# Performance work log

Measured on AMD Instinct MI355X. Metric: run time of the kernel, lower is better.

## Reference

```python
import jax, jax.numpy as jnp
import numpy as np
from jax import lax

B, C, H, W = 8, 64, 64, 64
C8 = C // 8
EPS = 1e-5


def setup_inputs() -> dict:
    key = jax.random.key(0)
    ks = jax.random.split(key, 10)
    s = lambda *sh: 0.02
    inp = {
        "x": jax.random.normal(ks[0], (B, C, H, W), dtype=jnp.float32),
        "conv_b_w": jax.random.normal(ks[1], (C8, C), dtype=jnp.float32) * 0.05,
        "conv_b_b": jnp.zeros((C8,), jnp.float32),
        "conv_c_w": jax.random.normal(ks[2], (C8, C), dtype=jnp.float32) * 0.05,
        "conv_c_b": jnp.zeros((C8,), jnp.float32),
        "conv_d_w": jax.random.normal(ks[3], (C, C), dtype=jnp.float32) * 0.05,
        "conv_d_b": jnp.zeros((C,), jnp.float32),
        "alpha": jnp.zeros((1,), jnp.float32) + 0.1,  # learned PAM scale
        "beta": jnp.zeros((1,), jnp.float32) + 0.1,   # learned CAM scale
        "conv_w": jax.random.normal(ks[4], (2 * C, C, 3, 3), dtype=jnp.float32) * 0.02,
        "conv_bias": jnp.zeros((2 * C,), jnp.float32),
        "bn_gamma": jnp.ones((2 * C,), jnp.float32),
        "bn_beta": jnp.zeros((2 * C,), jnp.float32),
    }
    return inp


def _conv1x1(x, w, b):
    # x: [B,C,H,W], w: [O,C] -> [B,O,H,W]
    return jnp.einsum('oc,bchw->bohw', w, x) + b[None, :, None, None]


def _forward(x, conv_b_w, conv_b_b, conv_c_w, conv_c_b, conv_d_w, conv_d_b,
             alpha, beta, conv_w, conv_bias, bn_gamma, bn_beta):
    b, c, h, w = x.shape
    n = h * w
    # ---- Position Attention Module ----
    feat_b = _conv1x1(x, conv_b_w, conv_b_b).reshape(b, C8, n)   # [B,C8,N]
    feat_c = _conv1x1(x, conv_c_w, conv_c_b).reshape(b, C8, n)   # [B,C8,N]
    # torch: bmm(feat_b^T [B,N,C8], feat_c [B,C8,N]) -> [B,N,N]
    attn_s = jax.nn.softmax(jnp.einsum('bcn,bcm->bnm', feat_b, feat_c), axis=-1)
    feat_d = _conv1x1(x, conv_d_w, conv_d_b).reshape(b, c, n)    # [B,C,N]
    # torch: bmm(feat_d, attn_s^T) -> out[b,c,n] = sum_m feat_d[b,c,m]*attn[b,n,m]
    feat_e = jnp.einsum('bcm,bnm->bcn', feat_d, attn_s).reshape(b, c, h, w)
    x = alpha[0] * feat_e + x
    # ---- Channel Attention Module ----
    fa = x.reshape(b, c, n)                                      # [B,C,N]
    att = jnp.einsum('bcn,bdn->bcd', fa, fa)                     # [B,C,C]
    att_new = jnp.max(att, axis=-1, keepdims=True) - att
    att = jax.nn.softmax(att_new, axis=-1)
    fe = jnp.einsum('bcd,bdn->bcn', att, fa).reshape(b, c, h, w)
    x = beta[0] * fe + x
    # ---- conv3x3 + BN (batch stats) + ReLU + maxpool(2,2,pad=(1,0)) ----
    out = lax.conv_general_dilated(x, conv_w, (1, 1), ((1, 1), (1, 1)),
                                   dimension_numbers=('NCHW', 'OIHW', 'NCHW'))
    out = out + conv_bias[None, :, None, None]
    mean = jnp.mean(out, axis=(0, 2, 3), keepdims=True)
    var = jnp.var(out, axis=(0, 2, 3), keepdims=True)
    out = (out - mean) * lax.rsqrt(var + EPS)
    out = out * bn_gamma[None, :, None, None] + bn_beta[None, :, None, None]
    out = jax.nn.relu(out)
    # MaxPool2d(kernel=2, stride=2, padding=(1,0)): -inf padding on height only
    out = lax.reduce_window(out, -jnp.inf, lax.max,
                            (1, 1, 2, 2), (1, 1, 2, 2),
                            ((0, 0), (0, 0), (1, 1), (0, 0)))
    return out


def reference(x, conv_b_w, conv_b_b, conv_c_w, conv_c_b, conv_d_w, conv_d_b,
              alpha, beta, conv_w, conv_bias, bn_gamma, bn_beta):
    return _forward(x, conv_b_w, conv_b_b, conv_c_w, conv_c_b, conv_d_w, conv_d_b,
                    alpha, beta, conv_w, conv_bias, bn_gamma, bn_beta)
```

## Files before the change

kernel.cpp:

```cpp
#include <hip/hip_runtime.h>

using f32x4  = __attribute__((ext_vector_type(4))) float;
using f32x16 = __attribute__((ext_vector_type(16))) float;
using bf16x8 = __attribute__((ext_vector_type(8))) short;
using u32x4  = __attribute__((ext_vector_type(4))) unsigned int;
using u32x2  = __attribute__((ext_vector_type(2))) unsigned int;
typedef unsigned short u16;

__device__ __forceinline__ u16 f2bf(float f) {
  unsigned u = __float_as_uint(f);
  unsigned r = (u + 0x7FFFu + ((u >> 16) & 1u)) >> 16;
  return (u16)r;
}

#if __has_builtin(__builtin_amdgcn_exp2f)
#define FAST_EXP2(x) __builtin_amdgcn_exp2f(x)
#else
#define FAST_EXP2(x) __expf(0.6931471805599453f * (x))
#endif

#define LOG2E 1.4426950408889634f

__device__ __forceinline__ void permswap32(unsigned& a, unsigned& b) {
  asm volatile("v_permlane32_swap_b32 %0, %1" : "+v"(a), "+v"(b));
}

__global__ void __launch_bounds__(256) k1_conv1x1(
    const float* __restrict__ x, const float* __restrict__ wB, const float* __restrict__ bB,
    const float* __restrict__ wC, const float* __restrict__ bC,
    const float* __restrict__ wD, const float* __restrict__ bD,
    u16* __restrict__ featBb, u16* __restrict__ featCb, u16* __restrict__ featD,
    const float* __restrict__ cw, u16* __restrict__ wb) {
  const int t = threadIdx.x;
  const int b = blockIdx.y;
  const int z = blockIdx.z;
  if (z == 2) {
    int gid = (b * 16 + blockIdx.x) * 256 + t;
#pragma unroll
    for (int k = 0; k < 3; ++k) {
      int F = gid + k * 32768;
      if (F < 73728) {
        int j = F & 7, lane = (F >> 3) & 63, T = F >> 9;
        int tap = T >> 4, g = (T >> 1) & 7, kc = T & 1;
        int l16 = lane & 15, quad = lane >> 4;
        int oc = g * 16 + l16, ic = kc * 32 + quad * 8 + j;
        wb[F] = f2bf(cw[(oc * 64 + ic) * 9 + tap]);
      }
    }
    return;
  }
  __shared__ float W[2560];
  __shared__ float Bias[40];
  const int n = blockIdx.x * 256 + t;
  if (z == 0) {
    for (int i = t; i < 2560; i += 256) {
      float v;
      if (i < 512) v = wB[i];
      else if (i < 1024) v = wC[i - 512];
      else v = wD[i - 1024];
      W[i] = v;
    }
    if (t < 8) Bias[t] = bB[t];
    else if (t < 16) Bias[t] = bC[t - 8];
    else if (t < 40) Bias[t] = bD[t - 16];
  } else {
    for (int i = t; i < 2560; i += 256) W[i] = wD[1536 + i];
    if (t < 40) Bias[t] = bD[24 + t];
  }
  __syncthreads();
  float xv[64];
#pragma unroll
  for (int c = 0; c < 64; ++c) xv[c] = x[((b * 64 + c) << 12) + n];
  if (z == 0) {
    float o[16];
#pragma unroll
    for (int k = 0; k < 16; ++k) {
      f32x4 s = {0.f, 0.f, 0.f, 0.f};
#pragma unroll
      for (int cq = 0; cq < 16; ++cq) {
        f32x4 wv = *(const f32x4*)&W[k * 64 + cq * 4];
        f32x4 xq = {xv[cq * 4], xv[cq * 4 + 1], xv[cq * 4 + 2], xv[cq * 4 + 3]};
        s += wv * xq;
      }
      o[k] = Bias[k] + s[0] + s[1] + s[2] + s[3];
    }
    int base = ((b << 12) + n) * 8;
    u32x4 pb, pc;
#pragma unroll
    for (int i = 0; i < 4; ++i) {
      pb[i] = (unsigned)f2bf(o[2 * i] * LOG2E) | ((unsigned)f2bf(o[2 * i + 1] * LOG2E) << 16);
      pc[i] = (unsigned)f2bf(o[8 + 2 * i]) | ((unsigned)f2bf(o[8 + 2 * i + 1]) << 16);
    }
    *(u32x4*)&featBb[base] = pb;
    *(u32x4*)&featCb[base] = pc;
#pragma unroll 4
    for (int k = 0; k < 24; ++k) {
      f32x4 s = {0.f, 0.f, 0.f, 0.f};
#pragma unroll
      for (int cq = 0; cq < 16; ++cq) {
        f32x4 wv = *(const f32x4*)&W[1024 + k * 64 + cq * 4];
        f32x4 xq = {xv[cq * 4], xv[cq * 4 + 1], xv[cq * 4 + 2], xv[cq * 4 + 3]};
        s += wv * xq;
      }
      float val = Bias[16 + k] + s[0] + s[1] + s[2] + s[3];
      featD[((b * 64 + k) << 12) + n] = f2bf(val);
    }
  } else {
#pragma unroll 4
    for (int k = 0; k < 40; ++k) {
      f32x4 s = {0.f, 0.f, 0.f, 0.f};
#pragma unroll
      for (int cq = 0; cq < 16; ++cq) {
        f32x4 wv = *(const f32x4*)&W[k * 64 + cq * 4];
        f32x4 xq = {xv[cq * 4], xv[cq * 4 + 1], xv[cq * 4 + 2], xv[cq * 4 + 3]};
        s += wv * xq;
      }
      float val = Bias[k] + s[0] + s[1] + s[2] + s[3];
      featD[((b * 64 + 24 + k) << 12) + n] = f2bf(val);
    }
  }
}

__global__ void __launch_bounds__(256) k2_pam_part(
    const u16* __restrict__ fBb, const u16* __restrict__ fCb, const u16* __restrict__ fD,
    u16* __restrict__ numPart, float* __restrict__ denPart) {
  __shared__ u16 Df[2][64 * 132];
  const int t = threadIdx.x, b = blockIdx.y, z = blockIdx.z;
  const int w = t >> 6, lane = t & 63, l32 = lane & 31, hi = lane >> 5;
  const int nb = blockIdx.x * 128 + w * 32;
  const int mz = z << 10;

  int srow[4], smo[4];
#pragma unroll
  for (int hh = 0; hh < 4; ++hh) {
    int idx = hh * 256 + t;
    srow[hh] = idx >> 4;
    smo[hh] = (idx & 15) << 3;
  }

  bf16x8 bq = (bf16x8)(short)0;
  if (hi == 0) bq = *(const bf16x8*)&fBb[(((b << 12) + nb + l32) << 3)];

  bf16x8 onesA = (bf16x8)(short)0;
  if (l32 == 0) onesA = (bf16x8)(short)0x3F80;

  f32x16 acc0 = (f32x16)(0.0f), acc1 = (f32x16)(0.0f), accd = (f32x16)(0.0f);

  u32x4 sreg[4];
#define K2_ISSUE(CH) {                                                        \
    int m0_ = mz + ((CH) << 7);                                               \
    _Pragma("unroll")                                                         \
    for (int hh = 0; hh < 4; ++hh)                                            \
      sreg[hh] = *(const u32x4*)&fD[((b * 64 + srow[hh]) << 12) + m0_ + smo[hh]]; }
#define K2_WRITE(BUF) {                                                       \
    _Pragma("unroll")                                                         \
    for (int hh = 0; hh < 4; ++hh)                                            \
      *(u32x4*)&Df[BUF][srow[hh] * 132 + smo[hh]] = sreg[hh]; }
#define K2_AF_LOAD(DST, CH) {                                                 \
    int m0_ = mz + ((CH) << 7);                                               \
    _Pragma("unroll")                                                         \
    for (int mt2 = 0; mt2 < 4; ++mt2) {                                       \
      bf16x8 a_ = (bf16x8)(short)0;                                           \
      if (hi == 0) a_ = *(const bf16x8*)&fCb[(((b << 12) + m0_ + mt2 * 32 + l32) << 3)]; \
      DST[mt2] = a_;                                                          \
    } }

  K2_ISSUE(0);
  K2_WRITE(0);
  bf16x8 afv[4], afn[4];
  K2_AF_LOAD(afv, 0);
  __syncthreads();

#pragma unroll 2
  for (int ch = 0; ch < 8; ++ch) {
    const int cur = ch & 1;
    if (ch < 7) K2_ISSUE(ch + 1);
    if (ch < 7) K2_AF_LOAD(afn, ch + 1);

    f32x16 sc = __builtin_amdgcn_mfma_f32_32x32x16_bf16(afv[0], bq, (f32x16)(0.0f), 0, 0, 0);
#pragma unroll
    for (int mt2 = 0; mt2 < 4; ++mt2) {
      f32x16 sn;
      if (mt2 < 3) sn = __builtin_amdgcn_mfma_f32_32x32x16_bf16(afv[mt2 + 1], bq, (f32x16)(0.0f), 0, 0, 0);
      unsigned u0[8];
#pragma unroll
      for (int i = 0; i < 8; ++i) {
        float e0 = FAST_EXP2(sc[2 * i]);
        float e1 = FAST_EXP2(sc[2 * i + 1]);
        u0[i] = __builtin_amdgcn_perm(__float_as_uint(e1), __float_as_uint(e0), 0x07060302u);
      }
      permswap32(u0[0], u0[2]); permswap32(u0[1], u0[3]);
      permswap32(u0[4], u0[6]); permswap32(u0[5], u0[7]);

      __builtin_amdgcn_s_setprio(1);
#pragma unroll
      for (int kc = 0; kc < 2; ++kc) {
        u32x4 q0 = {u0[4 * kc], u0[4 * kc + 1], u0[4 * kc + 2], u0[4 * kc + 3]};
        bf16x8 bv0 = *(bf16x8*)&q0;
        bf16x8 av0 = *(const bf16x8*)&Df[cur][(l32) * 132 + mt2 * 32 + kc * 16 + hi * 8];
        bf16x8 av1 = *(const bf16x8*)&Df[cur][(32 + l32) * 132 + mt2 * 32 + kc * 16 + hi * 8];
        acc0 = __builtin_amdgcn_mfma_f32_32x32x16_bf16(av0, bv0, acc0, 0, 0, 0);
        acc1 = __builtin_amdgcn_mfma_f32_32x32x16_bf16(av1, bv0, acc1, 0, 0, 0);
        accd = __builtin_amdgcn_mfma_f32_32x32x16_bf16(onesA, bv0, accd, 0, 0, 0);
      }
      __builtin_amdgcn_s_setprio(0);
      if (mt2 < 3) sc = sn;
    }

    if (ch < 7) {
      K2_WRITE(cur ^ 1);
#pragma unroll
      for (int mt2 = 0; mt2 < 4; ++mt2) afv[mt2] = afn[mt2];
    }
    __syncthreads();
  }
#undef K2_ISSUE
#undef K2_WRITE
#undef K2_AF_LOAD

  const int zb = z * 8 + b;
#pragma unroll
  for (int r = 0; r < 16; ++r) {
    int c = (r & 3) + ((r >> 2) << 3) + (hi << 2);
    numPart[((zb * 64 + c) << 12) + nb + l32] = (u16)(__float_as_uint(acc0[r]) >> 16);
    numPart[((zb * 64 + c + 32) << 12) + nb + l32] = (u16)(__float_as_uint(acc1[r]) >> 16);
  }
  if (hi == 0) denPart[(zb << 12) + nb + l32] = accd[0];
}

__global__ void __launch_bounds__(256) k3_gram(
    const u16* __restrict__ numPart, const float* __restrict__ denPart,
    const float* __restrict__ x, const float* __restrict__ alpha,
    float* __restrict__ x1, float* __restrict__ attPart) {
  __shared__ float X[64 * 132];
  __shared__ float Dinv[128];
  const int t = threadIdx.x, b = blockIdx.y, cx = blockIdx.x, zz = blockIdx.z;
  const int n0 = cx * 128;
  if (t < 128) {
    float den = 0.f;
#pragma unroll
    for (int z = 0; z < 4; ++z) den += denPart[(((z * 8 + b) << 12)) + n0 + t];
    Dinv[t] = alpha[0] / den;
  }
  __syncthreads();
  for (int idx = t; idx < 4096; idx += 256) {
    int row = idx >> 6, cp = (idx & 63) * 2;
    int gi = ((b * 64 + row) << 12) + n0 + cp;
    float num0 = 0.f, num1 = 0.f;
#pragma unroll
    for (int z = 0; z < 4; ++z) {
      unsigned v = *(const unsigned*)&numPart[(((z * 8 + b) * 64 + row) << 12) + n0 + cp];
      num0 += __uint_as_float(v << 16);
      num1 += __uint_as_float(v & 0xFFFF0000u);
    }
    float v0 = num0 * Dinv[cp] + x[gi];
    float v1 = num1 * Dinv[cp + 1] + x[gi + 1];
    X[row * 132 + cp] = v0;
    X[row * 132 + cp + 1] = v1;
    if (zz == 0) {
      x1[gi] = v0;
      x1[gi + 1] = v1;
    }
  }
  __syncthreads();
  const int cg = t >> 4, dg = t & 15;
  const int cbase = zz * 32 + cg * 2;
  f32x4 acc[2][4];
#pragma unroll
  for (int i = 0; i < 2; ++i)
#pragma unroll
    for (int k = 0; k < 4; ++k) acc[i][k] = (f32x4){0.f, 0.f, 0.f, 0.f};
  for (int nq0 = 0; nq0 < 32; ++nq0) {
    int nq = (nq0 + dg) & 31;
    f32x4 a[2], bb[4];
#pragma unroll
    for (int i = 0; i < 2; ++i) a[i] = *(const f32x4*)&X[(cbase + i) * 132 + nq * 4];
#pragma unroll
    for (int k = 0; k < 4; ++k) bb[k] = *(const f32x4*)&X[(dg * 4 + k) * 132 + nq * 4];
#pragma unroll
    for (int i = 0; i < 2; ++i)
#pragma unroll
      for (int k = 0; k < 4; ++k) acc[i][k] += a[i] * bb[k];
  }
#pragma unroll
  for (int i = 0; i < 2; ++i)
#pragma unroll
    for (int k = 0; k < 4; ++k) {
      f32x4 s = acc[i][k];
      attPart[((b * 32 + cx) * 64 + cbase + i) * 64 + dg * 4 + k] = s[0] + s[1] + s[2] + s[3];
    }
}

__global__ void __launch_bounds__(64) k4_softmax(const float* __restrict__ attPart, float* __restrict__ attP) {
  const int b = blockIdx.y, c = blockIdx.x, d = threadIdx.x;
  float v = 0.f;
  for (int p = 0; p < 32; ++p) v += attPart[((b * 32 + p) * 64 + c) * 64 + d];
  float mn = v;
#pragma unroll
  for (int off = 1; off < 64; off <<= 1) mn = fminf(mn, __shfl_xor(mn, off));
  float e = __expf(mn - v);
  float sum = e;
#pragma unroll
  for (int off = 1; off < 64; off <<= 1) sum += __shfl_xor(sum, off);
  attP[(b * 64 + c) * 64 + d] = e / sum;
}

__global__ void __launch_bounds__(256) k5_apply(
    const float* __restrict__ attP, const float* __restrict__ x1,
    const float* __restrict__ beta, u16* __restrict__ x2b) {
  __shared__ float A[64 * 68];
  const int t = threadIdx.x, b = blockIdx.y;
  for (int idx = t; idx < 4096; idx += 256) A[(idx >> 6) * 68 + (idx & 63)] = attP[(b << 12) + idx];
  __syncthreads();
  const int n = blockIdx.x * 32 + (t & 31);
  const int cq = t >> 5;
  const float bv = beta[0];
  float acc[8];
#pragma unroll
  for (int i = 0; i < 8; ++i) acc[i] = 0.f;
  const float* xcol = x1 + ((size_t)b << 18) + n;
#pragma unroll 4
  for (int dq = 0; dq < 16; ++dq) {
    float x0 = xcol[(size_t)(dq * 4 + 0) << 12];
    float x1v = xcol[(size_t)(dq * 4 + 1) << 12];
    float x2 = xcol[(size_t)(dq * 4 + 2) << 12];
    float x3 = xcol[(size_t)(dq * 4 + 3) << 12];
#pragma unroll
    for (int i = 0; i < 8; ++i) {
      const float* av = &A[(cq * 8 + i) * 68 + dq * 4];
      acc[i] += av[0] * x0 + av[1] * x1v + av[2] * x2 + av[3] * x3;
    }
  }
  u16* orow = x2b + ((((size_t)(b << 12) + n) << 6) + cq * 8);
  unsigned pk[4];
#pragma unroll
  for (int i = 0; i < 8; i += 2) {
    float v0 = bv * acc[i] + xcol[(size_t)(cq * 8 + i) << 12];
    float v1 = bv * acc[i + 1] + xcol[(size_t)(cq * 8 + i + 1) << 12];
    pk[i >> 1] = (unsigned)f2bf(v0) | ((unsigned)f2bf(v1) << 16);
  }
  *(u32x4*)&orow[0] = (u32x4){pk[0], pk[1], pk[2], pk[3]};
}

__global__ void __launch_bounds__(256) k6_mfma(const u16* __restrict__ x2b, const u16* __restrict__ wb,
                                               float* __restrict__ y, float* __restrict__ pstat2) {
  __shared__ u16 Xl[3 * 66 * 72];
  __shared__ float pp[4][64][2];
  const int t = threadIdx.x, b = blockIdx.y, h = blockIdx.x;
  for (int idx = t; idx < 3 * 66 * 8; idx += 256) {
    int r = idx / 528;
    int rem = idx - r * 528;
    int c = rem >> 3, icq = rem & 7;
    int gy = h - 1 + r, gx = c - 1;
    u32x4 v = {0u, 0u, 0u, 0u};
    if (gy >= 0 && gy < 64 && gx >= 0 && gx < 64)
      v = *(const u32x4*)&x2b[(((size_t)(b << 6 | gy) << 6) + gx) * 64 + icq * 8];
    *(u32x4*)&Xl[(r * 66 + c) * 72 + icq * 8] = v;
  }
  __syncthreads();
  const int w = t >> 6, lane = t & 63, quad = lane >> 4, l16 = lane & 15;
  const int mBase = (w & 1) * 64;
  const int og = (w & 1) * 4;
  const int nBase = (w >> 1) * 32;
  f32x4 acc[4][2];
#pragma unroll
  for (int ot = 0; ot < 4; ++ot)
#pragma unroll
    for (int nt = 0; nt < 2; ++nt) acc[ot][nt] = (f32x4){0.f, 0.f, 0.f, 0.f};
#pragma unroll 3
  for (int tap = 0; tap < 9; ++tap) {
    const int dy = tap / 3, dx = tap - dy * 3;
    bf16x8 af[4][2];
#pragma unroll
    for (int ot = 0; ot < 4; ++ot)
#pragma unroll
      for (int kc = 0; kc < 2; ++kc)
        af[ot][kc] = *(const bf16x8*)&wb[((((tap * 8 + og + ot) * 2 + kc) << 6) + lane) << 3];
#pragma unroll
    for (int nt = 0; nt < 2; ++nt) {
      const int prow = dy * 66 + nBase + nt * 16 + l16 + dx;
#pragma unroll
      for (int kc = 0; kc < 2; ++kc) {
        bf16x8 bv = *(const bf16x8*)&Xl[prow * 72 + kc * 32 + quad * 8];
#pragma unroll
        for (int ot = 0; ot < 4; ++ot)
          acc[ot][nt] = __builtin_amdgcn_mfma_f32_16x16x32_bf16(af[ot][kc], bv, acc[ot][nt], 0, 0, 0);
      }
    }
  }
#pragma unroll
  for (int ot = 0; ot < 4; ++ot)
#pragma unroll
    for (int nt = 0; nt < 2; ++nt)
#pragma unroll
      for (int r = 0; r < 4; ++r) {
        int oc = mBase + ot * 16 + quad * 4 + r;
        int pix = nBase + nt * 16 + l16;
        y[((b * 128 + oc) << 12) + (h << 6) + pix] = acc[ot][nt][r];
      }
  float bs[4][4], bss[4][4];
#pragma unroll
  for (int ot = 0; ot < 4; ++ot)
#pragma unroll
    for (int r = 0; r < 4; ++r) {
      float v0 = acc[ot][0][r], v1 = acc[ot][1][r];
      bs[ot][r] = v0 + v1;
      bss[ot][r] = v0 * v0 + v1 * v1;
    }
#pragma unroll
  for (int off = 1; off < 16; off <<= 1) {
#pragma unroll
    for (int ot = 0; ot < 4; ++ot)
#pragma unroll
      for (int r = 0; r < 4; ++r) {
        bs[ot][r] += __shfl_xor(bs[ot][r], off);
        bss[ot][r] += __shfl_xor(bss[ot][r], off);
      }
  }
  if (l16 == 0) {
#pragma unroll
    for (int ot = 0; ot < 4; ++ot)
#pragma unroll
      for (int r = 0; r < 4; ++r) {
        int ocl = ot * 16 + quad * 4 + r;
        pp[w][ocl][0] = bs[ot][r];
        pp[w][ocl][1] = bss[ot][r];
      }
  }
  __syncthreads();
  {
    int oc = t >> 1, st = t & 1;
    float v = (oc < 64) ? (pp[0][oc][st] + pp[2][oc][st])
                        : (pp[1][oc - 64][st] + pp[3][oc - 64][st]);
    pstat2[(oc * 2 + st) * 512 + (b << 6) + h] = v;
  }
}

__global__ void __launch_bounds__(256) k8_pool(const float* __restrict__ y, const float* __restrict__ pstat2,
                                               const float* __restrict__ gamma, const float* __restrict__ bbeta,
                                               float* __restrict__ out) {
  const int bc = blockIdx.x;
  const int ch = bc & 127;
  float s = 0.f, ss = 0.f;
  for (int i = threadIdx.x; i < 512; i += 256) {
    s += pstat2[ch * 1024 + i];
    ss += pstat2[ch * 1024 + 512 + i];
  }
#pragma unroll
  for (int off = 1; off < 64; off <<= 1) { s += __shfl_xor(s, off); ss += __shfl_xor(ss, off); }
  __shared__ float rs[4], rss[4];
  if ((threadIdx.x & 63) == 0) { rs[threadIdx.x >> 6] = s; rss[threadIdx.x >> 6] = ss; }
  __syncthreads();
  const float S = rs[0] + rs[1] + rs[2] + rs[3];
  const float SS = rss[0] + rss[1] + rss[2] + rss[3];
  const float mean = S * (1.f / 32768.f);
  const float var = SS * (1.f / 32768.f) - mean * mean;
  const float sc = gamma[ch] * rsqrtf(var + 1e-5f);
  const float sh = bbeta[ch] - mean * sc;
  const float* p = y + (bc << 12);
  float* op = out + bc * (33 * 32);
  for (int i = threadIdx.x; i < 33 * 32; i += 256) {
    int oh = i >> 5, ow = i & 31;
    int r0 = 2 * oh - 1, r1 = 2 * oh;
    float m = 0.f;
    if (r0 >= 0) {
      m = fmaxf(m, p[r0 * 64 + 2 * ow] * sc + sh);
      m = fmaxf(m, p[r0 * 64 + 2 * ow + 1] * sc + sh);
    }
    if (r1 <= 63) {
      m = fmaxf(m, p[r1 * 64 + 2 * ow] * sc + sh);
      m = fmaxf(m, p[r1 * 64 + 2 * ow + 1] * sc + sh);
    }
    op[i] = m;
  }
}

extern "C" void kernel_launch(void* const* d_in, const int* in_sizes, int n_in,
                              void* d_out, int out_size, void* d_ws, size_t ws_size,
                              hipStream_t stream) {
  const float* x      = (const float*)d_in[0];
  const float* wB     = (const float*)d_in[1];
  const float* bB     = (const float*)d_in[2];
  const float* wC     = (const float*)d_in[3];
  const float* bC     = (const float*)d_in[4];
  const float* wD     = (const float*)d_in[5];
  const float* bD     = (const float*)d_in[6];
  const float* alpha  = (const float*)d_in[7];
  const float* beta   = (const float*)d_in[8];
  const float* cw     = (const float*)d_in[9];
  const float* gamma  = (const float*)d_in[11];
  const float* bnbeta = (const float*)d_in[12];

  char* ws = (char*)d_ws;
  u16*   featBb  = (u16*)  (ws + 0);
  u16*   featCb  = (u16*)  (ws + 524288);
  u16*   fDb     = (u16*)  (ws + 1048576);
  u16*   x2b     = (u16*)  (ws + 0);
  float* x1      = (float*)(ws + 5242880);
  u16*   numPart = (u16*)  (ws + 13631488);
  float* y       = (float*)(ws + 13631488);
  float* denPart = (float*)(ws + 30408704);
  float* attPart = (float*)(ws + 30932992);
  float* pstat2  = (float*)(ws + 30932992);
  float* attP    = (float*)(ws + 35127296);
  u16*   wb      = (u16*)  (ws + 35258368);
  float* outp    = (float*)d_out;

  k1_conv1x1<<<dim3(16, 8, 3), 256, 0, stream>>>(x, wB, bB, wC, bC, wD, bD, featBb, featCb, fDb, cw, wb);
  k2_pam_part<<<dim3(32, 8, 4), 256, 0, stream>>>(featBb, featCb, fDb, numPart, denPart);
  k3_gram<<<dim3(32, 8, 2), 256, 0, stream>>>(numPart, denPart, x, alpha, x1, attPart);
  k4_softmax<<<dim3(64, 8), 64, 0, stream>>>(attPart, attP);
  k5_apply<<<dim3(128, 8), 256, 0, stream>>>(attP, x1, beta, x2b);
  k6_mfma<<<dim3(64, 8), 256, 0, stream>>>(x2b, wb, y, pstat2);
  k8_pool<<<dim3(1024), 256, 0, stream>>>(y, pstat2, gamma, bnbeta, outp);
}
```

Before: 182.6 us.

## Remove CAM softmax kernel via atomic gram reduction and softmax in apply kernel

The gram kernel now atomically adds its per-chunk partial C×C products straight into a single attention buffer, which the first kernel zeroes. This replaces the separate partial buffer and the 32-way reduction. The standalone softmax kernel is removed. Each apply block now recomputes the min-subtract softmax on its shared-memory copy of the 64×64 matrix. This saves one launch and the partial-buffer traffic, but adds float atomics (making the sum order nondeterministic) and repeats the softmax work in all 128 apply blocks per batch.

```diff
diff --git a/kernel.cpp b/kernel.cpp
--- a/kernel.cpp
+++ b/kernel.cpp
@@ -30,12 +30,13 @@
     const float* __restrict__ wC, const float* __restrict__ bC,
     const float* __restrict__ wD, const float* __restrict__ bD,
     u16* __restrict__ featBb, u16* __restrict__ featCb, u16* __restrict__ featD,
-    const float* __restrict__ cw, u16* __restrict__ wb) {
+    const float* __restrict__ cw, u16* __restrict__ wb, float* __restrict__ att) {
   const int t = threadIdx.x;
   const int b = blockIdx.y;
   const int z = blockIdx.z;
   if (z == 2) {
     int gid = (b * 16 + blockIdx.x) * 256 + t;
+    att[gid] = 0.f;
 #pragma unroll
     for (int k = 0; k < 3; ++k) {
       int F = gid + k * 32768;
@@ -231,7 +232,7 @@
 __global__ void __launch_bounds__(256) k3_gram(
     const u16* __restrict__ numPart, const float* __restrict__ denPart,
     const float* __restrict__ x, const float* __restrict__ alpha,
-    float* __restrict__ x1, float* __restrict__ attPart) {
+    float* __restrict__ x1, float* __restrict__ att) {
   __shared__ float X[64 * 132];
   __shared__ float Dinv[128];
   const int t = threadIdx.x, b = blockIdx.y, cx = blockIdx.x, zz = blockIdx.z;
@@ -287,30 +288,37 @@
 #pragma unroll
     for (int k = 0; k < 4; ++k) {
       f32x4 s = acc[i][k];
-      attPart[((b * 32 + cx) * 64 + cbase + i) * 64 + dg * 4 + k] = s[0] + s[1] + s[2] + s[3];
-    }
-}
-
-__global__ void __launch_bounds__(64) k4_softmax(const float* __restrict__ attPart, float* __restrict__ attP) {
-  const int b = blockIdx.y, c = blockIdx.x, d = threadIdx.x;
-  float v = 0.f;
-  for (int p = 0; p < 32; ++p) v += attPart[((b * 32 + p) * 64 + c) * 64 + d];
-  float mn = v;
-#pragma unroll
-  for (int off = 1; off < 64; off <<= 1) mn = fminf(mn, __shfl_xor(mn, off));
-  float e = __expf(mn - v);
-  float sum = e;
-#pragma unroll
-  for (int off = 1; off < 64; off <<= 1) sum += __shfl_xor(sum, off);
-  attP[(b * 64 + c) * 64 + d] = e / sum;
+      atomicAdd(&att[((b * 64 + cbase + i) << 6) + dg * 4 + k], s[0] + s[1] + s[2] + s[3]);
+    }
 }
 
 __global__ void __launch_bounds__(256) k5_apply(
-    const float* __restrict__ attP, const float* __restrict__ x1,
+    const float* __restrict__ att, const float* __restrict__ x1,
     const float* __restrict__ beta, u16* __restrict__ x2b) {
   __shared__ float A[64 * 68];
   const int t = threadIdx.x, b = blockIdx.y;
-  for (int idx = t; idx < 4096; idx += 256) A[(idx >> 6) * 68 + (idx & 63)] = attP[(b << 12) + idx];
+  for (int idx = t; idx < 4096; idx += 256) A[(idx >> 6) * 68 + (idx & 63)] = att[(b << 12) + idx];
+  __syncthreads();
+  {
+    const int r = t >> 2, sub = t & 3;
+    float mn = 1e30f;
+#pragma unroll
+    for (int d = 0; d < 16; ++d) mn = fminf(mn, A[r * 68 + sub * 16 + d]);
+    mn = fminf(mn, __shfl_xor(mn, 1));
+    mn = fminf(mn, __shfl_xor(mn, 2));
+    float sm = 0.f;
+#pragma unroll
+    for (int d = 0; d < 16; ++d) {
+      float e = __expf(mn - A[r * 68 + sub * 16 + d]);
+      A[r * 68 + sub * 16 + d] = e;
+      sm += e;
+    }
+    sm += __shfl_xor(sm, 1);
+    sm += __shfl_xor(sm, 2);
+    float inv = 1.f / sm;
+#pragma unroll
+    for (int d = 0; d < 16; ++d) A[r * 68 + sub * 16 + d] *= inv;
+  }
   __syncthreads();
   const int n = blockIdx.x * 32 + (t & 31);
   const int cq = t >> 5;
@@ -500,17 +508,15 @@
   u16*   numPart = (u16*)  (ws + 13631488);
   float* y       = (float*)(ws + 13631488);
   float* denPart = (float*)(ws + 30408704);
-  float* attPart = (float*)(ws + 30932992);
   float* pstat2  = (float*)(ws + 30932992);
-  float* attP    = (float*)(ws + 35127296);
+  float* att     = (float*)(ws + 35127296);
   u16*   wb      = (u16*)  (ws + 35258368);
   float* outp    = (float*)d_out;
 
-  k1_conv1x1<<<dim3(16, 8, 3), 256, 0, stream>>>(x, wB, bB, wC, bC, wD, bD, featBb, featCb, fDb, cw, wb);
+  k1_conv1x1<<<dim3(16, 8, 3), 256, 0, stream>>>(x, wB, bB, wC, bC, wD, bD, featBb, featCb, fDb, cw, wb, att);
   k2_pam_part<<<dim3(32, 8, 4), 256, 0, stream>>>(featBb, featCb, fDb, numPart, denPart);
-  k3_gram<<<dim3(32, 8, 2), 256, 0, stream>>>(numPart, denPart, x, alpha, x1, attPart);
-  k4_softmax<<<dim3(64, 8), 64, 0, stream>>>(attPart, attP);
-  k5_apply<<<dim3(128, 8), 256, 0, stream>>>(attP, x1, beta, x2b);
+  k3_gram<<<dim3(32, 8, 2), 256, 0, stream>>>(numPart, denPart, x, alpha, x1, att);
+  k5_apply<<<dim3(128, 8), 256, 0, stream>>>(att, x1, beta, x2b);
   k6_mfma<<<dim3(64, 8), 256, 0, stream>>>(x2b, wb, y, pstat2);
   k8_pool<<<dim3(1024), 256, 0, stream>>>(y, pstat2, gamma, bnbeta, outp);
 }
```

New measurement: 196.7 us. 7.7% more time.
